# Optimization experiments

Measured on AMD Instinct MI355X. Metric: run time of the kernel, lower is better.

The kernel has to match this reference:

```python
import jax, jax.numpy as jnp
import numpy as np

MOLS = 64
ATOMS = 256
N = MOLS * ATOMS
K_GB = 32
K_GNN = 16
HID = 128
OFFSET = 0.009            # GB dielectric offset (nm)
ALPHA, BETA, GAMMA = 1.0, 0.8, 4.85  # OBC2 coefficients
EPS_FACTOR = 138.935456   # Coulomb constant, kJ*nm/(mol*e^2)
PREF = -EPS_FACTOR * (1.0 - 1.0 / 78.5)


def _edges(key, k_neigh):
    # random intra-molecule neighbors, no self loops (mimics radius-graph structure)
    src = jnp.repeat(jnp.arange(N), k_neigh)
    off = jax.random.randint(key, (N * k_neigh,), 1, ATOMS)
    dst = (src // ATOMS) * ATOMS + (src % ATOMS + off) % ATOMS
    return jnp.stack([src, dst]).astype(jnp.int32)


def setup_inputs() -> dict:
    key = jax.random.key(0)
    ks = jax.random.split(key, 8)
    pos = (jax.random.uniform(ks[0], (N, 3), jnp.float32) * 1.5)
    q = jax.random.uniform(ks[1], (N, 1), jnp.float32) - 0.5
    rad = 0.15 + 0.05 * jax.random.uniform(ks[2], (N, 1), jnp.float32)
    scl = 0.8 + 0.2 * jax.random.uniform(ks[3], (N, 1), jnp.float32)
    rest = jax.random.uniform(ks[4], (N, 4), jnp.float32)
    atom_features = jnp.concatenate([q, rad, scl, rest], axis=1)
    batch = jnp.repeat(jnp.arange(MOLS), ATOMS).astype(jnp.int32)
    edge_index = _edges(ks[5], K_GB)
    gnn_edge_index = _edges(ks[6], K_GNN)

    def lin(k, fi, fo):
        return (jax.random.normal(k, (fi, fo), jnp.float32) / np.float32(np.sqrt(fi)),
                jnp.zeros((fo,), jnp.float32))
    kw = jax.random.split(ks[7], 6)
    i1_w1, i1_b1 = lin(kw[0], 2 * 2 + 1, HID)
    i1_w2, i1_b2 = lin(kw[1], HID, HID)
    i2_w1, i2_b1 = lin(kw[2], 2 * HID + 1, HID)
    i2_w2, i2_b2 = lin(kw[3], HID, HID)
    i3_w1, i3_b1 = lin(kw[4], 2 * HID + 1, HID)
    i3_w2, i3_b2 = lin(kw[5], HID, 1)
    return dict(pos=pos, atom_features=atom_features, batch=batch,
                edge_index=edge_index, gnn_edge_index=gnn_edge_index,
                i1_w1=i1_w1, i1_b1=i1_b1, i1_w2=i1_w2, i1_b2=i1_b2,
                i2_w1=i2_w1, i2_b1=i2_b1, i2_w2=i2_w2, i2_b2=i2_b2,
                i3_w1=i3_w1, i3_b1=i3_b1, i3_w2=i3_w2, i3_b2=i3_b2)


def _dist(pos, ei):
    d2 = jnp.sum((pos[ei[0]] - pos[ei[1]]) ** 2, axis=1)
    return jnp.sqrt(d2 + 1e-12)


def _gb_energies(pos, feats, ei):
    # GBNeck_interaction (Born radii via HCT descreening integral, OBC2 rescale)
    # followed by GBNeck_energies (pairwise GB + self energy), per-atom [N,1]
    n = pos.shape[0]
    src, dst = ei[0], ei[1]
    d = _dist(pos, ei)
    q, radius, scale = feats[:, 0], feats[:, 1], feats[:, 2]
    rho = radius - OFFSET
    sr_j = (scale * rho)[src]
    rho_i = rho[dst]
    U = d + sr_j
    L = jnp.maximum(rho_i, jnp.abs(d - sr_j))
    I = 0.5 * (1.0 / L - 1.0 / U
               + 0.25 * (d - sr_j ** 2 / d) * (1.0 / U ** 2 - 1.0 / L ** 2)
               + 0.5 * jnp.log(L / U) / d)
    I = jnp.where(rho_i < U, I, 0.0)
    Isum = jax.ops.segment_sum(I, dst, num_segments=n)
    psi = Isum * rho
    B = 1.0 / (1.0 / rho - jnp.tanh(ALPHA * psi - BETA * psi ** 2 + GAMMA * psi ** 3) / radius)
    Bi, Bj = B[dst], B[src]
    f_gb = jnp.sqrt(d ** 2 + Bi * Bj * jnp.exp(-d ** 2 / (4.0 * Bi * Bj)))
    e_pair = 0.5 * PREF * q[dst] * q[src] / f_gb  # 0.5: edges are double counted
    e = 0.5 * PREF * q ** 2 / B + jax.ops.segment_sum(e_pair, dst, num_segments=n)
    return e[:, None]


def _in_layer(x, ei, d, w1, b1, w2, b2):
    # IN_layer_all_swish_2pass: edge MLP on [x_i || x_j || d] + scatter-add
    n = x.shape[0]
    m = jnp.concatenate([x[ei[0]], x[ei[1]], d[:, None]], axis=1)
    h = jax.nn.silu(m @ w1 + b1)
    return jax.ops.segment_sum(h @ w2 + b2, ei[1], num_segments=n)


def _energies_all(pos, feats, ei, gei,
                  i1_w1, i1_b1, i1_w2, i1_b2,
                  i2_w1, i2_b1, i2_w2, i2_b2,
                  i3_w1, i3_b1, i3_w2, i3_b2):
    e_gb = _gb_energies(pos, feats, ei)
    d_gnn = _dist(pos, gei)
    x = jax.nn.silu(_in_layer(feats[:, :2], gei, d_gnn, i1_w1, i1_b1, i1_w2, i1_b2))
    x = jax.nn.silu(_in_layer(x, gei, d_gnn, i2_w1, i2_b1, i2_w2, i2_b2))
    x = _in_layer(x, gei, d_gnn, i3_w1, i3_b1, i3_w2, i3_b2)
    return e_gb + x


def reference(pos, atom_features, batch, edge_index, gnn_edge_index,
              i1_w1, i1_b1, i1_w2, i1_b2,
              i2_w1, i2_b1, i2_w2, i2_b2,
              i3_w1, i3_b1, i3_w2, i3_b2):
    ws = (i1_w1, i1_b1, i1_w2, i1_b2, i2_w1, i2_b1, i2_w2, i2_b2,
          i3_w1, i3_b1, i3_w2, i3_b2)
    efun = lambda p: _energies_all(p, atom_features, edge_index, gnn_edge_index, *ws)
    energies, vjp = jax.vjp(efun, pos)  # [N,1]
    (gpos,) = vjp(jnp.ones_like(energies))
    forces = -gpos
    energy = jax.ops.segment_sum(energies[:, 0], batch, num_segments=MOLS)[:, None]
    return energy, forces
```

## Files before the change

kernel.cpp:

```cpp
#include <hip/hip_runtime.h>
#include <hip/hip_bf16.h>

#define NATOMS 16384
#define MOLS   64
#define ATOMSM 256
#define EGB    524288
#define EGNN   262144
#define HID    128
#define NH     (NATOMS*HID)

#define OFFSETC 0.009f
#define ALPHAC  1.0f
#define BETAC   0.8f
#define GAMMAC  4.85f
#define PREFC   (-138.935456f*(1.0f-1.0f/78.5f))

typedef __hip_bfloat16 bf;
typedef __attribute__((ext_vector_type(8))) short bf8v;
typedef __attribute__((ext_vector_type(4))) float f4v;
typedef unsigned int uint;

__device__ __forceinline__ float b2f(bf x){ return __bfloat162float(x); }
__device__ __forceinline__ bf f2b(float x){ return __float2bfloat16(x); }
__device__ __forceinline__ short f2s(float x){ bf h = f2b(x); return *(short*)&h; }
// ... 53 lines not shown
    short* __restrict__ A3at, short* __restrict__ A3bt,
    short* __restrict__ rA2a, short* __restrict__ rA2b,
    short* __restrict__ rA3a, short* __restrict__ rA3b,
    short* __restrict__ rC1, short* __restrict__ rC2,
    const float* __restrict__ feat, const float* __restrict__ A1,
    bf* __restrict__ u1, bf* __restrict__ v1,
    const float* __restrict__ pos, const int* __restrict__ ei,
    float* __restrict__ Isum,
    const int* __restrict__ gei, float* __restrict__ dgnn, int* __restrict__ cnt)
{
    int tid = threadIdx.x;
    if (blockIdx.x < 64){
        int gid = blockIdx.x*256 + tid;
        int j = gid >> 7, k = gid & 127;
        C1t[gid]  = f2s(C1[k*HID+j]);
        C2t[gid]  = f2s(C2[k*HID+j]);
        A2at[gid] = f2s(A2[k*HID+j]);
        A2bt[gid] = f2s(A2[(HID+k)*HID+j]);
        A3at[gid] = f2s(A3[k*HID+j]);
        A3bt[gid] = f2s(A3[(HID+k)*HID+j]);
        rA2a[gid] = f2s(A2[gid]);
        rA2b[gid] = f2s(A2[HID*HID+gid]);
        rA3a[gid] = f2s(A3[gid]);
        rA3b[gid] = f2s(A3[HID*HID+gid]);
        rC1[gid]  = f2s(C1[gid]);
        rC2[gid]  = f2s(C2[gid]);
    } else if (blockIdx.x < 4160){
        int gid2 = (blockIdx.x-64)*256 + tid;
        int i = gid2 >> 6, k2 = (gid2 & 63)*2;
        float q = feat[7*i+0], r = feat[7*i+1];
        float u0 = q*A1[k2]         + r*A1[HID+k2];
        float u1v= q*A1[k2+1]       + r*A1[HID+k2+1];
        float v0 = q*A1[2*HID+k2]   + r*A1[3*HID+k2];
        float v1v= q*A1[2*HID+k2+1] + r*A1[3*HID+k2+1];
        ushort2 uu, vv;
        uu.x = (unsigned short)f2s(u0); uu.y = (unsigned short)f2s(u1v);
        vv.x = (unsigned short)f2s(v0); vv.y = (unsigned short)f2s(v1v);
        *(ushort2*)((short*)u1 + (size_t)i*HID + k2) = uu;
        *(ushort2*)((short*)v1 + (size_t)i*HID + k2) = vv;
    } else if (blockIdx.x < 4672){
        __shared__ float sPx[256], sPy[256], sPz[256], sRho[256], sSr[256];
        __shared__ float sI[256];
        int bb = blockIdx.x - 4160;
        int mbase = (bb >> 3) * 256;
        {
            int i = mbase + tid;
            sPx[tid]=pos[3*i]; sPy[tid]=pos[3*i+1]; sPz[tid]=pos[3*i+2];
            float rad = feat[7*i+1], sc = feat[7*i+2];
            float rho = rad - OFFSETC;
            sRho[tid]=rho; sSr[tid]=sc*rho;
            sI[tid]=0.f;
        }
        __syncthreads();
        int T = bb*256 + tid;
        int s = T >> 3, p = T & 7;
        int sl = s & 255;
        int e0 = s*32 + p*4;
        float px = sPx[sl], py = sPy[sl], pz = sPz[sl];
        float sr = sSr[sl];
        float srr = sr*sr;
        const int* dP = ei + EGB;
        int4 d4 = *(const int4*)(dP + e0);
        int dls[4] = {d4.x&255, d4.y&255, d4.z&255, d4.w&255};
#pragma unroll
        for (int j=0;j<4;j++){
            int dl = dls[j];
            float dx = px - sPx[dl];
            float dy = py - sPy[dl];
            float dz = pz - sPz[dl];
            float d2 = dx*dx+dy*dy+dz*dz + 1e-12f;
            float rd = frsq(d2);
            float d  = d2*rd;
            float rho_i = sRho[dl];
            float U = d + sr;
            if (rho_i < U){
                float L = fmaxf(rho_i, fabsf(d - sr));
                float invU = frcp(U), invL = frcp(L);
                float I = 0.5f*invL - 0.5f*invU
                        + 0.125f*(d - srr*rd)*(invU*invU - invL*invL)
                        + 0.25f*__logf(L*invU)*rd;
                atomicAdd(&sI[dl], I);
            }
        }
        __syncthreads();
        atomicAdd(&Isum[mbase + tid], sI[tid]);
    } else {
        int e = (blockIdx.x-4672)*256 + tid;
        int s = gei[e], dd = gei[EGNN+e];
        float dx = pos[3*s+0] - pos[3*dd+0];
        float dy = pos[3*s+1] - pos[3*dd+1];
        float dz = pos[3*s+2] - pos[3*dd+2];
        dgnn[e] = fsqrt(dx*dx+dy*dy+dz*dz + 1e-12f);
        atomicAdd(&cnt[dd], 1);
    }
}

__global__ __launch_bounds__(256) void k_B(
    const float* __restrict__ feat, const float* __restrict__ Isum,
    float* __restrict__ Bv, float* __restrict__ cB, float* __restrict__ gB,
    float* __restrict__ egb,
    const int* __restrict__ cnt, int* __restrict__ rptr,
    const int* __restrict__ gei, const float* __restrict__ dgnn,
    int* __restrict__ csr, int2* __restrict__ csr2)
{
    int t = threadIdx.x;
    if (blockIdx.x < 64){
        int i = blockIdx.x*256 + t;
        float q   = feat[7*i+0];
        float rad = feat[7*i+1];
        float rho = rad - OFFSETC;
        float psi = Isum[i]*rho;
        float u = psi*(ALPHAC + psi*(-BETAC + GAMMAC*psi));
        float tt = tanhf(u);
        float rrad = frcp(rad);
        float B = frcp(frcp(rho) - tt*rrad);
        Bv[i] = B;
        float du = ALPHAC + psi*(-2.0f*BETAC + 3.0f*GAMMAC*psi);
        cB[i] = B*B*((1.0f-tt*tt)*rrad)*du*rho;
        float Cs = 0.5f*PREFC*q*q;
        float rB = frcp(B);
        egb[i] = Cs*rB;
        gB[i]  = -Cs*rB*rB;
    } else {
        __shared__ int sc[256];
        __shared__ int lcur[256];
        int m = blockIdx.x - 64;
        int c = cnt[m*256+t];
        sc[t] = c; __syncthreads();
        for (int off=1; off<256; off<<=1){
            int x = (t>=off) ? sc[t-off] : 0;
            __syncthreads();
            sc[t] += x;
            __syncthreads();
        }
        int exl = sc[t] - c;
        rptr[m*256+t] = m*4096 + exl;
        lcur[t] = exl;
        __syncthreads();
        int e0 = m*4096;
        for (int j=t; j<4096; j+=256){
            int e = e0 + j;
            int dl = gei[EGNN+e] & 255;
            float d = dgnn[e];
            int p = atomicAdd(&lcur[dl], 1);
            int idx = e0 + p;
            csr[idx] = e;
            int2 rec; rec.x = (e >> 4) << 8;
            rec.y = __float_as_int(d);
            csr2[idx] = rec;
        }
    }
}

__global__ __launch_bounds__(256) void k_gbC(
    const float* __restrict__ pos, const float* __restrict__ feat,
    const int* __restrict__ ei, const float* __restrict__ Bv,
    float* __restrict__ egb, float* __restrict__ gdgb, float* __restrict__ gB)
{
    __shared__ float sPx[256], sPy[256], sPz[256], sB[256], sQf[256];
    __shared__ float sE[256], sG[256];
    int tid = threadIdx.x;
    int mbase = (blockIdx.x >> 3) * 256;
    {
        int i = mbase + tid;
        sPx[tid]=pos[3*i]; sPy[tid]=pos[3*i+1]; sPz[tid]=pos[3*i+2];
        sB[tid]=Bv[i]; sQf[tid]=feat[7*i+0];
        sE[tid]=0.f; sG[tid]=0.f;
    }
    __syncthreads();
    int T = blockIdx.x*256 + tid;
    int s = T >> 3, p = T & 7;
    int sl = s & 255;
    int e0 = s*32 + p*4;
    float px = sPx[sl], py = sPy[sl], pz = sPz[sl];
    float qs = sQf[sl];
    float Bs = sB[sl];
    float gsrc = 0.f;
    const int* dP = ei + EGB;
    int4 d4 = *(const int4*)(dP + e0);
    int dls[4] = {d4.x&255, d4.y&255, d4.z&255, d4.w&255};
#pragma unroll
    for (int j=0;j<4;j++){
        int dl = dls[j];
        float dx = px - sPx[dl];
        float dy = py - sPy[dl];
        float dz = pz - sPz[dl];
        float d2 = dx*dx+dy*dy+dz*dz + 1e-12f;
        float d  = d2*frsq(d2);
        float Bd = sB[dl];
        float C = 0.5f*PREFC*sQf[dl]*qs;
        float P = Bd*Bs;
        float qq = 0.25f*d2*frcp(P);
        float ex = __expf(-qq);
        float f2 = d2 + P*ex;
        float rf = frsq(f2);
        float f3i = rf*rf*rf;
        gdgb[e0+j] = -C*d*(1.f - 0.25f*ex)*f3i;
        float common = -C*ex*(1.f + qq)*0.5f*f3i;
        atomicAdd(&sE[dl], C*rf);
        atomicAdd(&sG[dl], common*Bs);
        gsrc += common*Bd;
    }
    gsrc += __shfl_xor(gsrc,1);
    gsrc += __shfl_xor(gsrc,2);
    gsrc += __shfl_xor(gsrc,4);
    if (p==0) atomicAdd(&sG[sl], gsrc);
    __syncthreads();
    atomicAdd(&egb[mbase + tid], sE[tid]);
    atomicAdd(&gB[mbase + tid],  sG[tid]);
}

__global__ __launch_bounds__(256) void k_gbE(
    const float* __restrict__ pos, const float* __restrict__ feat,
    const int* __restrict__ ei, const float* __restrict__ cB,
    const float* __restrict__ gB,
    const float* __restrict__ gdgb, float* __restrict__ grad)
{
    __shared__ float sPx[256], sPy[256], sPz[256], sRho[256], sSr[256], sCg[256];
    __shared__ float sGx[256], sGy[256], sGz[256];
    int tid = threadIdx.x;
    int mbase = (blockIdx.x >> 3) * 256;
    {
        int i = mbase + tid;
        sPx[tid]=pos[3*i]; sPy[tid]=pos[3*i+1]; sPz[tid]=pos[3*i+2];
        float rad = feat[7*i+1], sc = feat[7*i+2];
        float rho = rad - OFFSETC;
        sRho[tid]=rho; sSr[tid]=sc*rho;
        sCg[tid]=cB[i]*gB[i];
        sGx[tid]=0.f; sGy[tid]=0.f; sGz[tid]=0.f;
    }
    __syncthreads();
    int T = blockIdx.x*256 + tid;
    int s = T >> 3, p = T & 7;
    int sl = s & 255;
    int e0 = s*32 + p*4;
    float px = sPx[sl], py = sPy[sl], pz = sPz[sl];
    float sr = sSr[sl];
    float srr = sr*sr;
    float gx=0.f, gy=0.f, gz=0.f;
    const int* dP = ei + EGB;
    int4 d4 = *(const int4*)(dP + e0);
    int dls[4] = {d4.x&255, d4.y&255, d4.z&255, d4.w&255};
#pragma unroll
    for (int j=0;j<4;j++){
        int dl = dls[j];
        float dx = px - sPx[dl];
        float dy = py - sPy[dl];
        float dz = pz - sPz[dl];
        float d2 = dx*dx+dy*dy+dz*dz + 1e-12f;
        float rd = frsq(d2);
        float d  = d2*rd;
        float rd2 = rd*rd;
        float rho_i = sRho[dl];
        float U = d + sr;
        float gd = gdgb[e0+j];
        if (rho_i < U){
            float aa = fabsf(d - sr);
            float L, Lp;
            if (rho_i >= aa){ L = rho_i; Lp = 0.f; }
            else { L = aa; Lp = (d >= sr) ? 1.f : -1.f; }
            float invU = frcp(U), invL = frcp(L);
            float invU2=invU*invU, invL2=invL*invL;
            float dIdd = -0.5f*Lp*invL2 + 0.5f*invU2
                + 0.125f*(1.f + srr*rd2)*(invU2 - invL2)
                + 0.125f*(d - srr*rd)*(2.f*Lp*invL2*invL - 2.f*invU2*invU)
                + 0.25f*((Lp*invL - invU)*rd - __logf(L*invU)*rd2);
            gd += sCg[dl]*dIdd;
        }
        float c = gd*rd;
        gx += c*dx; gy += c*dy; gz += c*dz;
        atomicAdd(&sGx[dl], -c*dx);
        atomicAdd(&sGy[dl], -c*dy);
        atomicAdd(&sGz[dl], -c*dz);
    }
    gx += __shfl_xor(gx,1); gx += __shfl_xor(gx,2); gx += __shfl_xor(gx,4);
    gy += __shfl_xor(gy,1); gy += __shfl_xor(gy,2); gy += __shfl_xor(gy,4);
    gz += __shfl_xor(gz,1); gz += __shfl_xor(gz,2); gz += __shfl_xor(gz,4);
    if (p==0){
        atomicAdd(&sGx[sl], gx);
        atomicAdd(&sGy[sl], gy);
        atomicAdd(&sGz[sl], gz);
    }
    __syncthreads();
    int i = mbase + tid;
    atomicAdd(&grad[3*i+0], sGx[tid]);
    atomicAdd(&grad[3*i+1], sGy[tid]);
    atomicAdd(&grad[3*i+2], sGz[tid]);
}


template<bool WSDS>
__device__ __forceinline__ void edge_fwd_wave(
    int dst, int lane,
    const int2* __restrict__ csr2, const int* __restrict__ rptr, const int* __restrict__ cnt,
    const uint* __restrict__ u, const uint* __restrict__ v,
    const float* __restrict__ wdp, const float* __restrict__ bb,
    uint* __restrict__ Hs, uint* __restrict__ Sds)
{
    int n = cnt[dst], r0 = rptr[dst];
    float2 wd = *(const float2*)&wdp[2*lane];
    float2 b2 = *(const float2*)&bb[2*lane];
    uint vp = v[dst*64 + lane];
    float base0 = lo2f(vp) + b2.x;
    float base1 = hi2f(vp) + b2.y;
    float h0=0.f,h1=0.f,e0a=0.f,e1a=0.f;
    for (int j0=0; j0<n; j0+=64){
        int m = n - j0; if (m > 64) m = 64;
        int rx = 0, ry = 0;
        if (lane < m){ int2 rc = csr2[r0+j0+lane]; rx = rc.x; ry = rc.y; }
#pragma unroll 2
        for (int j=0;j<m;j++){
            int off = __builtin_amdgcn_readlane(rx, j);
            float d  = __uint_as_float((unsigned)__builtin_amdgcn_readlane(ry, j));
            uint up = *(const uint*)((const char*)u + off + 4*lane);
            float a0 = fmaf(d, wd.x, base0 + lo2f(up));
            float a1 = fmaf(d, wd.y, base1 + hi2f(up));
            float s0 = sigf(a0), s1 = sigf(a1);
            float p0 = a0*s0, p1 = a1*s1;
            h0 += p0; h1 += p1;
            if (WSDS){
                e0a = fmaf(s0, 1.f + a0 - p0, e0a);
                e1a = fmaf(s1, 1.f + a1 - p1, e1a);
            }
        }
    }
    Hs[dst*64+lane] = pack2(h0,h1);
    if (WSDS) Sds[dst*64+lane] = pack2(e0a,e1a);
}

__global__ __launch_bounds__(256,8) void k_edge_fwd0(
    const int2* __restrict__ csr2, const int* __restrict__ rptr, const int* __restrict__ cnt,
    const uint* __restrict__ u, const uint* __restrict__ v,
    const float* __restrict__ wdp, const float* __restrict__ bb,
    uint* __restrict__ Hs)
{
    int lane = threadIdx.x & 63, wid = threadIdx.x >> 6;
    int dst = blockIdx.x*4 + wid;
    edge_fwd_wave<false>(dst, lane, csr2, rptr, cnt, u, v, wdp, bb, Hs, nullptr);
}

__global__ __launch_bounds__(256,8) void k_edge_fwd1(
    const int2* __restrict__ csr2, const int* __restrict__ rptr, const int* __restrict__ cnt,
    const uint* __restrict__ u, const uint* __restrict__ v,
    const float* __restrict__ wdp, const float* __restrict__ bb,
    uint* __restrict__ Hs, uint* __restrict__ Sds)
{
    int lane = threadIdx.x & 63, wid = threadIdx.x >> 6;
    int dst = blockIdx.x*4 + wid;
    edge_fwd_wave<true>(dst, lane, csr2, rptr, cnt, u, v, wdp, bb, Hs, Sds);
}

__global__ __launch_bounds__(256,4) void k_l3(
    const int2* __restrict__ csr2, const int* __restrict__ rptr, const int* __restrict__ cnt,
    const int* __restrict__ gei, const float* __restrict__ dgnn,
    const uint* __restrict__ u, const uint* __restrict__ v,
    const float* __restrict__ A3, const float* __restrict__ B3,
    const float* __restrict__ C3, const float* __restrict__ D3,
    uint* __restrict__ Gd, float* __restrict__ x3,
    uint* __restrict__ Gs, float* __restrict__ gdg)
{
    int lane = threadIdx.x & 63, wid = threadIdx.x >> 6;
    const float* wdp = A3 + 256*HID;
    if (blockIdx.x < NATOMS/4){
        int dst = blockIdx.x*4 + wid;
        int n = cnt[dst], r0 = rptr[dst];
        float2 wd = *(const float2*)&wdp[2*lane];
        float2 b2 = *(const float2*)&B3[2*lane];
        float2 ck = *(const float2*)&C3[2*lane];
        uint vp = v[dst*64 + lane];
        float base0 = lo2f(vp) + b2.x;
        float base1 = hi2f(vp) + b2.y;
        float h0=0.f,h1=0.f,e0a=0.f,e1a=0.f;
        for (int j0=0; j0<n; j0+=64){
            int m = n - j0; if (m > 64) m = 64;
            int rx = 0, ry = 0;
            if (lane < m){ int2 rc = csr2[r0+j0+lane]; rx = rc.x; ry = rc.y; }
#pragma unroll 2
            for (int j=0;j<m;j++){
                int off = __builtin_amdgcn_readlane(rx, j);
                float d  = __uint_as_float((unsigned)__builtin_amdgcn_readlane(ry, j));
                uint up = *(const uint*)((const char*)u + off + 4*lane);
                float a0 = fmaf(d, wd.x, base0 + lo2f(up));
                float a1 = fmaf(d, wd.y, base1 + hi2f(up));
                float s0 = sigf(a0), s1 = sigf(a1);
                float p0 = a0*s0, p1 = a1*s1;
                h0 += p0; h1 += p1;
                e0a = fmaf(s0, 1.f + a0 - p0, e0a);
                e1a = fmaf(s1, 1.f + a1 - p1, e1a);
            }
        }
        Gd[dst*64+lane] = pack2(ck.x*e0a, ck.y*e1a);
        float px = waveRed(ck.x*h0 + ck.y*h1);
        if (lane==0) x3[dst] = px + (float)n*D3[0];
    } else {
        int s = (blockIdx.x - NATOMS/4)*4 + wid;
        int doff = 0, dbit = 0;
        if (lane < 16){
            doff = gei[EGNN + s*16 + lane] << 8;
            dbit = __float_as_int(dgnn[s*16+lane]);
        }
        float2 wd = *(const float2*)&wdp[2*lane];
        float2 b2 = *(const float2*)&B3[2*lane];
        float2 ck = *(const float2*)&C3[2*lane];
        uint up = u[s*64 + lane];
        float us0 = lo2f(up) + b2.x;
        float us1 = hi2f(up) + b2.y;
        float cw0 = ck.x*wd.x, cw1 = ck.y*wd.y;
        float gs0=0.f, gs1=0.f;
        float A[16];
#pragma unroll
        for (int t=0;t<16;t++){
            int off = __builtin_amdgcn_readlane(doff, t);
            float d = __uint_as_float((unsigned)__builtin_amdgcn_readlane(dbit, t));
            uint vp = *(const uint*)((const char*)v + off + 4*lane);
            float a0 = fmaf(d, wd.x, us0 + lo2f(vp));
            float a1 = fmaf(d, wd.y, us1 + hi2f(vp));
            float s0 = sigf(a0), s1 = sigf(a1);
            float p0 = a0*s0, p1 = a1*s1;
            float dv0 = s0*(1.f + a0 - p0);
            float dv1 = s1*(1.f + a1 - p1);
            gs0 += dv0; gs1 += dv1;
            A[t] = fmaf(dv1, cw1, dv0*cw0);
        }
        Gs[s*64+lane] = pack2(ck.x*gs0, ck.y*gs1);
        float tot = red16(A, lane);
        if (lane < 32 && !(lane & 1)) gdg[s*16 + (lane>>1)] = tot;
    }
}

__global__ __launch_bounds__(256,4) void k_bwd_src(
    const int* __restrict__ gei, const float* __restrict__ dgnn,
    const uint* __restrict__ u, const uint* __restrict__ v,
    const float* __restrict__ wdp, const float* __restrict__ bb,
    const uint* __restrict__ gH,
    uint* __restrict__ Gs, float* __restrict__ gdg)
{
    int lane = threadIdx.x & 63, wid = threadIdx.x >> 6;
    int s = blockIdx.x*4 + wid;
    int doff = 0, dbit = 0;
    if (lane < 16){
        doff = gei[EGNN + s*16 + lane] << 8;
        dbit = __float_as_int(dgnn[s*16+lane]);
    }
    float gold = gdg[s*16 + ((lane>>1)&15)];
    float2 wd = *(const float2*)&wdp[2*lane];
    float2 b2 = *(const float2*)&bb[2*lane];
    uint up = u[s*64 + lane];
    float us0 = lo2f(up) + b2.x;
    float us1 = hi2f(up) + b2.y;
    float gs0=0.f, gs1=0.f;
    float A[16];
#pragma unroll
    for (int t=0;t<16;t++){
        int off = __builtin_amdgcn_readlane(doff, t);
        float d = __uint_as_float((unsigned)__builtin_amdgcn_readlane(dbit, t));
        uint vp = *(const uint*)((const char*)v + off + 4*lane);
        uint gp = *(const uint*)((const char*)gH + off + 4*lane);
        float a0 = fmaf(d, wd.x, us0 + lo2f(vp));
        float a1 = fmaf(d, wd.y, us1 + hi2f(vp));
        float s0 = sigf(a0), s1 = sigf(a1);
        float p0 = a0*s0, p1 = a1*s1;
        float ga0 = s0*(1.f + a0 - p0) * lo2f(gp);
        float ga1 = s1*(1.f + a1 - p1) * hi2f(gp);
        gs0 += ga0; gs1 += ga1;
        A[t] = fmaf(ga1, wd.y, ga0*wd.x);
    }
    if (Gs) Gs[s*64+lane] = pack2(gs0, gs1);
    float tot = red16(A, lane);
    if (lane < 32 && !(lane & 1)) gdg[s*16 + (lane>>1)] = gold + tot;
}

__global__ __launch_bounds__(256) void k_node_fwd_uv_mfma(
    const short* __restrict__ Hs, const int* __restrict__ cnt,
    const short* __restrict__ Ct, const float* __restrict__ D,
    const short* __restrict__ Aat, const short* __restrict__ Abt,
    bf* __restrict__ dsz, bf* __restrict__ u, bf* __restrict__ v)
{
    __shared__ short sx[64*HID];
    int lane = threadIdx.x & 63, w = threadIdx.x >> 6;
    int m0 = blockIdx.x*64 + w*16;
    int ar = lane & 15, kg = lane >> 4;
    bf8v af[4];
#pragma unroll
    for (int s=0;s<4;s++) af[s] = *(const bf8v*)&Hs[(size_t)(m0+ar)*HID + s*32 + kg*8];
    f4v acc[8];
#pragma unroll
    for (int nt=0;nt<8;nt++){
        acc[nt] = (f4v){0.f,0.f,0.f,0.f};
        const short* bp = Ct + (nt*16+ar)*HID + kg*8;
#pragma unroll
        for (int s=0;s<4;s++){
            bf8v bv = *(const bf8v*)(bp + s*32);
            acc[nt] = __builtin_amdgcn_mfma_f32_16x16x32_bf16(af[s], bv, acc[nt], 0,0,0);
        }
    }
    float cn[4];
#pragma unroll
    for (int r=0;r<4;r++) cn[r] = (float)cnt[m0 + kg*4 + r];
#pragma unroll
    for (int nt=0;nt<8;nt++){
        int j = nt*16 + ar;
        float Dj = D[j];
#pragma unroll
        for (int r=0;r<4;r++){
            int m = m0 + kg*4 + r;
            float zv = acc[nt][r] + cn[r]*Dj;
            float sg = sigf(zv);
            dsz[(size_t)m*HID + j] = f2b(sg*(1.f + zv*(1.f - sg)));
            sx[(w*16 + kg*4 + r)*HID + j] = f2s(zv*sg);
        }
    }
    __syncthreads();
#pragma unroll
    for (int s=0;s<4;s++) af[s] = *(const bf8v*)&sx[(w*16+ar)*HID + s*32 + kg*8];
    f4v au[8], av[8];
#pragma unroll
    for (int nt=0;nt<8;nt++){
        au[nt] = (f4v){0.f,0.f,0.f,0.f};
        av[nt] = (f4v){0.f,0.f,0.f,0.f};
        const short* bpa = Aat + (nt*16+ar)*HID + kg*8;
        const short* bpb = Abt + (nt*16+ar)*HID + kg*8;
#pragma unroll
        for (int s=0;s<4;s++){
            bf8v ba = *(const bf8v*)(bpa + s*32);
            bf8v bb = *(const bf8v*)(bpb + s*32);
            au[nt] = __builtin_amdgcn_mfma_f32_16x16x32_bf16(af[s], ba, au[nt], 0,0,0);
            av[nt] = __builtin_amdgcn_mfma_f32_16x16x32_bf16(af[s], bb, av[nt], 0,0,0);
        }
    }
#pragma unroll
    for (int nt=0;nt<8;nt++){
        int j = nt*16 + ar;
#pragma unroll
        for (int r=0;r<4;r++){
            int m = m0 + kg*4 + r;
            u[(size_t)m*HID + j] = f2b(au[nt][r]);
            v[(size_t)m*HID + j] = f2b(av[nt][r]);
        }
    }
}

__global__ __launch_bounds__(256) void k_gx_node_bwd_mfma(
    const short* __restrict__ Gs, const short* __restrict__ Gd,
    const short* __restrict__ gHin, const short* __restrict__ Sds,
    const short* __restrict__ Ra, const short* __restrict__ Rb,
    const bf* __restrict__ dsz, const short* __restrict__ Rc,
    bf* __restrict__ gHout)
{
    __shared__ short st[64*HID];
    int lane = threadIdx.x & 63, w = threadIdx.x >> 6;
    int m0 = blockIdx.x*64 + w*16;
    int ar = lane & 15, kg = lane >> 4;
    bf8v as_[4], ad_[4];
#pragma unroll
    for (int s=0;s<4;s++)
        as_[s] = *(const bf8v*)&Gs[(size_t)(m0+ar)*HID + s*32 + kg*8];
    if (Sds){
#pragma unroll
        for (int s=0;s<4;s++){
            bf8v g = *(const bf8v*)&gHin[(size_t)(m0+ar)*HID + s*32 + kg*8];
            bf8v sd = *(const bf8v*)&Sds[(size_t)(m0+ar)*HID + s*32 + kg*8];
            bf8v r;
#pragma unroll
            for (int i=0;i<8;i++) r[i] = f2s(s2f(g[i])*s2f(sd[i]));
            ad_[s] = r;
        }
    } else {
#pragma unroll
        for (int s=0;s<4;s++)
            ad_[s] = *(const bf8v*)&Gd[(size_t)(m0+ar)*HID + s*32 + kg*8];
    }
    f4v acc[8];
#pragma unroll
    for (int nt=0;nt<8;nt++){
        acc[nt] = (f4v){0.f,0.f,0.f,0.f};
        const short* bpa = Ra + (nt*16+ar)*HID + kg*8;
        const short* bpb = Rb + (nt*16+ar)*HID + kg*8;
#pragma unroll
        for (int s=0;s<4;s++){
            bf8v ba = *(const bf8v*)(bpa + s*32);
            bf8v bb = *(const bf8v*)(bpb + s*32);
            acc[nt] = __builtin_amdgcn_mfma_f32_16x16x32_bf16(as_[s], ba, acc[nt], 0,0,0);
            acc[nt] = __builtin_amdgcn_mfma_f32_16x16x32_bf16(ad_[s], bb, acc[nt], 0,0,0);
        }
    }
#pragma unroll
    for (int nt=0;nt<8;nt++){
        int j = nt*16 + ar;
#pragma unroll
        for (int r=0;r<4;r++){
            int m = m0 + kg*4 + r;
            float t = acc[nt][r] * b2f(dsz[(size_t)m*HID + j]);
            st[(w*16 + kg*4 + r)*HID + j] = f2s(t);
        }
    }
    __syncthreads();
    bf8v af[4];
#pragma unroll
    for (int s=0;s<4;s++) af[s] = *(const bf8v*)&st[(w*16+ar)*HID + s*32 + kg*8];
    f4v a2[8];
#pragma unroll
    for (int nt=0;nt<8;nt++){
        a2[nt] = (f4v){0.f,0.f,0.f,0.f};
        const short* bp = Rc + (nt*16+ar)*HID + kg*8;
#pragma unroll
        for (int s=0;s<4;s++){
            bf8v bc = *(const bf8v*)(bp + s*32);
            a2[nt] = __builtin_amdgcn_mfma_f32_16x16x32_bf16(af[s], bc, a2[nt], 0,0,0);
        }
    }
#pragma unroll
    for (int nt=0;nt<8;nt++){
        int j = nt*16 + ar;
#pragma unroll
        for (int r=0;r<4;r++){
            gHout[(size_t)(m0 + kg*4 + r)*HID + j] = f2b(a2[nt][r]);
        }
    }
}

__global__ __launch_bounds__(256) void k_out(
    const float* __restrict__ pos, const int* __restrict__ gei,
    const int* __restrict__ csr, const int* __restrict__ rptr, const int* __restrict__ cnt,
    const float* __restrict__ dgnn, const float* __restrict__ gdg,
    const float* __restrict__ grad,
    const float* __restrict__ egb, const float* __restrict__ x3,
    float* __restrict__ out)
{
    int tid = threadIdx.x;
    if (blockIdx.x < 512){
        float* fout = out + MOLS;
        int T = blockIdx.x*256 + tid;
        int i = T >> 3, p = T & 7;
        float px = pos[3*i+0], py = pos[3*i+1], pz = pos[3*i+2];
        float ax=0.f, ay=0.f, az=0.f;
        for (int j=p;j<16;j+=8){
            int e = i*16 + j;
            int o = gei[EGNN+e];
            float c = gdg[e]*frcp(dgnn[e]);
            ax += c*(px - pos[3*o+0]);
            ay += c*(py - pos[3*o+1]);
            az += c*(pz - pos[3*o+2]);
        }
        int n = cnt[i], r0 = rptr[i];
        for (int j=p;j<n;j+=8){
            int e = csr[r0+j];
            int o = e >> 4;
            float c = gdg[e]*frcp(dgnn[e]);
            ax += c*(px - pos[3*o+0]);
            ay += c*(py - pos[3*o+1]);
            az += c*(pz - pos[3*o+2]);
        }
        ax += __shfl_xor(ax,1); ax += __shfl_xor(ax,2); ax += __shfl_xor(ax,4);
        ay += __shfl_xor(ay,1); ay += __shfl_xor(ay,2); ay += __shfl_xor(ay,4);
        az += __shfl_xor(az,1); az += __shfl_xor(az,2); az += __shfl_xor(az,4);
        if (p==0){
            fout[3*i+0] = -(grad[3*i+0] + ax);
            fout[3*i+1] = -(grad[3*i+1] + ay);
            fout[3*i+2] = -(grad[3*i+2] + az);
        }
    } else {
        __shared__ float red[4];
        int m = blockIdx.x - 512;
        int i = m*ATOMSM + tid;
        float en = egb[i] + x3[i];
        float v = waveRed(en);
        int wave = tid>>6, lane = tid&63;
        if (lane==0) red[wave] = v;
        __syncthreads();
        if (tid==0) out[m] = red[0]+red[1]+red[2]+red[3];
    }
}

extern "C" void kernel_launch(void* const* d_in, const int* in_sizes, int n_in,
                              void* d_out, int out_size, void* d_ws, size_t ws_size,
                              hipStream_t stream)
{
    const float* pos  = (const float*)d_in[0];
    const float* feat = (const float*)d_in[1];
    const int* ei  = (const int*)d_in[3];
    const int* gei = (const int*)d_in[4];
    const float* A1f = (const float*)d_in[5];  const float* B1f = (const float*)d_in[6];
    const float* C1f = (const float*)d_in[7];  const float* D1f = (const float*)d_in[8];
    const float* A2f = (const float*)d_in[9];  const float* B2f = (const float*)d_in[10];
    const float* C2f = (const float*)d_in[11]; const float* D2f = (const float*)d_in[12];
    const float* A3f = (const float*)d_in[13]; const float* B3f = (const float*)d_in[14];
    const float* C3f = (const float*)d_in[15]; const float* D3f = (const float*)d_in[16];

    float* w = (float*)d_ws;
    size_t off = 0;
    auto nxt = [&](size_t n)->float*{ float* p = w + off; off += (n + 255) & ~(size_t)255; return p; };
    float* Isum = nxt(NATOMS);
    int*   cnt  = (int*)nxt(NATOMS);
    float* grad = nxt(3*NATOMS);
    float* Bv = nxt(NATOMS); float* cB = nxt(NATOMS);
    float* gB = nxt(NATOMS); float* egb = nxt(NATOMS); float* x3 = nxt(NATOMS);
    int*   rptr = (int*)nxt(NATOMS);
    int*   csr  = (int*)nxt(EGNN);
    int2*  csr2 = (int2*)nxt((size_t)EGNN*2);
    float* dgnn = nxt(EGNN); float* gdgnn = nxt(EGNN); float* gdgb = nxt(EGB);
    bf* dsz1 = (bf*)nxt(NH/2); bf* dsz2 = (bf*)nxt(NH/2);
    bf* Hs1 = (bf*)nxt(NH/2); bf* Hs2 = (bf*)nxt(NH/2);
    bf* Gs3 = (bf*)nxt(NH/2); bf* Gd3 = (bf*)nxt(NH/2);
    bf* Sds2 = (bf*)nxt(NH/2);
    bf* u1 = (bf*)nxt(NH/2); bf* v1 = (bf*)nxt(NH/2);
    bf* u2 = (bf*)nxt(NH/2); bf* v2 = (bf*)nxt(NH/2);
    bf* v3 = (bf*)nxt(NH/2);
    short* C1t  = (short*)nxt(8192); short* C2t  = (short*)nxt(8192);
    short* A2at = (short*)nxt(8192); short* A2bt = (short*)nxt(8192);
    short* A3at = (short*)nxt(8192); short* A3bt = (short*)nxt(8192);
    short* rA2a = (short*)nxt(8192); short* rA2b = (short*)nxt(8192);
    short* rA3a = (short*)nxt(8192); short* rA3b = (short*)nxt(8192);
    short* rC1  = (short*)nxt(8192); short* rC2  = (short*)nxt(8192);
    bf* u3  = Hs1;
    bf* gH2 = Hs2;
    bf* Gs2 = Gs3;
    bf* gH1 = u3;

    hipMemsetAsync(Isum, 0, (size_t)5*NATOMS*sizeof(float), stream);

    k_A<<<64 + NH/512 + 512 + EGNN/256, 256, 0, stream>>>(
        A2f, C1f, A3f, C2f,
        C1t, C2t, A2at, A2bt, A3at, A3bt, rA2a, rA2b, rA3a, rA3b, rC1, rC2,
        feat, A1f, u1, v1,
        pos, ei, Isum, gei, dgnn, cnt);

    k_B<<<128,256,0,stream>>>(feat, Isum, Bv, cB, gB, egb, cnt, rptr,
                              gei, dgnn, csr, csr2);

    k_edge_fwd0<<<NATOMS/4,256,0,stream>>>(csr2, rptr, cnt, (const uint*)u1, (const uint*)v1,
                                           A1f+4*HID, B1f, (uint*)Hs1);
    k_gbC<<<512,256,0,stream>>>(pos, feat, ei, Bv, egb, gdgb, gB);
    k_node_fwd_uv_mfma<<<NATOMS/64,256,0,stream>>>((const short*)Hs1, cnt, C1t, D1f,
                                                   A2at, A2bt, dsz1, u2, v2);
    k_edge_fwd1<<<NATOMS/4,256,0,stream>>>(csr2, rptr, cnt, (const uint*)u2, (const uint*)v2,
                                           A2f+256*HID, B2f, (uint*)Hs2, (uint*)Sds2);
    k_gbE<<<512,256,0,stream>>>(pos, feat, ei, cB, gB, gdgb, grad);
    k_node_fwd_uv_mfma<<<NATOMS/64,256,0,stream>>>((const short*)Hs2, cnt, C2t, D2f,
                                                   A3at, A3bt, dsz2, u3, v3);

    k_l3<<<2*(NATOMS/4),256,0,stream>>>(csr2, rptr, cnt, gei, dgnn,
                                        (const uint*)u3, (const uint*)v3,
                                        A3f, B3f, C3f, D3f,
                                        (uint*)Gd3, x3, (uint*)Gs3, gdgnn);

    k_gx_node_bwd_mfma<<<NATOMS/64,256,0,stream>>>((const short*)Gs3, (const short*)Gd3,
        (const short*)nullptr, (const short*)nullptr, rA3a, rA3b, dsz2, rC2, gH2);
    k_bwd_src<<<NATOMS/4,256,0,stream>>>(gei, dgnn, (const uint*)u2, (const uint*)v2,
                                         A2f+256*HID, B2f, (const uint*)gH2,
                                         (uint*)Gs2, gdgnn);
    k_gx_node_bwd_mfma<<<NATOMS/64,256,0,stream>>>((const short*)Gs2, (const short*)nullptr,
        (const short*)gH2, (const short*)Sds2, rA2a, rA2b, dsz1, rC1, gH1);
    k_bwd_src<<<NATOMS/4,256,0,stream>>>(gei, dgnn, (const uint*)u1, (const uint*)v1,
                                         A1f+4*HID, B1f, (const uint*)gH1,
                                         (uint*)nullptr, gdgnn);

    k_out<<<576,256,0,stream>>>(pos, gei, csr, rptr, cnt, dgnn, gdgnn,
                                grad, egb, x3, (float*)d_out);
}
```

Baseline: 328.9 us.

## Merge GB pair kernels into GNN edge kernels via block-range dispatch

Folds the GB energy kernel (k_gbC) into the layer-1 edge-forward launch and the GB gradient kernel (k_gbE) into the layer-2 edge-forward launch. Each combined kernel sends its first 512 blocks to the GB work and the rest to the edge work, so the independent tasks run side by side and two launches go away. The change also raises the gather-loop unroll from 2 to 8, builds row pointers from an unsigned offset, and raises the min-waves hint from 4 to 6 in k_l3 and k_bwd_src. Possible costs are higher register use from the fused shared-memory branches and the larger unroll, plus register spills under the tighter launch bounds.

```diff
diff --git a/kernel.cpp b/kernel.cpp
--- a/kernel.cpp
+++ b/kernel.cpp
@@ -229,143 +229,6 @@
     }
 }
 
-__global__ __launch_bounds__(256) void k_gbC(
-    const float* __restrict__ pos, const float* __restrict__ feat,
-    const int* __restrict__ ei, const float* __restrict__ Bv,
-    float* __restrict__ egb, float* __restrict__ gdgb, float* __restrict__ gB)
-{
-    __shared__ float sPx[256], sPy[256], sPz[256], sB[256], sQf[256];
-    __shared__ float sE[256], sG[256];
-    int tid = threadIdx.x;
-    int mbase = (blockIdx.x >> 3) * 256;
-    {
-        int i = mbase + tid;
-        sPx[tid]=pos[3*i]; sPy[tid]=pos[3*i+1]; sPz[tid]=pos[3*i+2];
-        sB[tid]=Bv[i]; sQf[tid]=feat[7*i+0];
-        sE[tid]=0.f; sG[tid]=0.f;
-    }
-    __syncthreads();
-    int T = blockIdx.x*256 + tid;
-    int s = T >> 3, p = T & 7;
-    int sl = s & 255;
-    int e0 = s*32 + p*4;
-    float px = sPx[sl], py = sPy[sl], pz = sPz[sl];
-    float qs = sQf[sl];
-    float Bs = sB[sl];
-    float gsrc = 0.f;
-    const int* dP = ei + EGB;
-    int4 d4 = *(const int4*)(dP + e0);
-    int dls[4] = {d4.x&255, d4.y&255, d4.z&255, d4.w&255};
-#pragma unroll
-    for (int j=0;j<4;j++){
-        int dl = dls[j];
-        float dx = px - sPx[dl];
-        float dy = py - sPy[dl];
-        float dz = pz - sPz[dl];
-        float d2 = dx*dx+dy*dy+dz*dz + 1e-12f;
-        float d  = d2*frsq(d2);
-        float Bd = sB[dl];
-        float C = 0.5f*PREFC*sQf[dl]*qs;
-        float P = Bd*Bs;
-        float qq = 0.25f*d2*frcp(P);
-        float ex = __expf(-qq);
-        float f2 = d2 + P*ex;
-        float rf = frsq(f2);
-        float f3i = rf*rf*rf;
-        gdgb[e0+j] = -C*d*(1.f - 0.25f*ex)*f3i;
-        float common = -C*ex*(1.f + qq)*0.5f*f3i;
-        atomicAdd(&sE[dl], C*rf);
-        atomicAdd(&sG[dl], common*Bs);
-        gsrc += common*Bd;
-    }
-    gsrc += __shfl_xor(gsrc,1);
-    gsrc += __shfl_xor(gsrc,2);
-    gsrc += __shfl_xor(gsrc,4);
-    if (p==0) atomicAdd(&sG[sl], gsrc);
-    __syncthreads();
-    atomicAdd(&egb[mbase + tid], sE[tid]);
-    atomicAdd(&gB[mbase + tid],  sG[tid]);
-}
-
-__global__ __launch_bounds__(256) void k_gbE(
-    const float* __restrict__ pos, const float* __restrict__ feat,
-    const int* __restrict__ ei, const float* __restrict__ cB,
-    const float* __restrict__ gB,
-    const float* __restrict__ gdgb, float* __restrict__ grad)
-{
-    __shared__ float sPx[256], sPy[256], sPz[256], sRho[256], sSr[256], sCg[256];
-    __shared__ float sGx[256], sGy[256], sGz[256];
-    int tid = threadIdx.x;
-    int mbase = (blockIdx.x >> 3) * 256;
-    {
-        int i = mbase + tid;
-        sPx[tid]=pos[3*i]; sPy[tid]=pos[3*i+1]; sPz[tid]=pos[3*i+2];
-        float rad = feat[7*i+1], sc = feat[7*i+2];
-        float rho = rad - OFFSETC;
-        sRho[tid]=rho; sSr[tid]=sc*rho;
-        sCg[tid]=cB[i]*gB[i];
-        sGx[tid]=0.f; sGy[tid]=0.f; sGz[tid]=0.f;
-    }
-    __syncthreads();
-    int T = blockIdx.x*256 + tid;
-    int s = T >> 3, p = T & 7;
-    int sl = s & 255;
-    int e0 = s*32 + p*4;
-    float px = sPx[sl], py = sPy[sl], pz = sPz[sl];
-    float sr = sSr[sl];
-    float srr = sr*sr;
-    float gx=0.f, gy=0.f, gz=0.f;
-    const int* dP = ei + EGB;
-    int4 d4 = *(const int4*)(dP + e0);
-    int dls[4] = {d4.x&255, d4.y&255, d4.z&255, d4.w&255};
-#pragma unroll
-    for (int j=0;j<4;j++){
-        int dl = dls[j];
-        float dx = px - sPx[dl];
-        float dy = py - sPy[dl];
-        float dz = pz - sPz[dl];
-        float d2 = dx*dx+dy*dy+dz*dz + 1e-12f;
-        float rd = frsq(d2);
-        float d  = d2*rd;
-        float rd2 = rd*rd;
-        float rho_i = sRho[dl];
-        float U = d + sr;
-        float gd = gdgb[e0+j];
-        if (rho_i < U){
-            float aa = fabsf(d - sr);
-            float L, Lp;
-            if (rho_i >= aa){ L = rho_i; Lp = 0.f; }
-            else { L = aa; Lp = (d >= sr) ? 1.f : -1.f; }
-            float invU = frcp(U), invL = frcp(L);
-            float invU2=invU*invU, invL2=invL*invL;
-            float dIdd = -0.5f*Lp*invL2 + 0.5f*invU2
-                + 0.125f*(1.f + srr*rd2)*(invU2 - invL2)
-                + 0.125f*(d - srr*rd)*(2.f*Lp*invL2*invL - 2.f*invU2*invU)
-                + 0.25f*((Lp*invL - invU)*rd - __logf(L*invU)*rd2);
-            gd += sCg[dl]*dIdd;
-        }
-        float c = gd*rd;
-        gx += c*dx; gy += c*dy; gz += c*dz;
-        atomicAdd(&sGx[dl], -c*dx);
-        atomicAdd(&sGy[dl], -c*dy);
-        atomicAdd(&sGz[dl], -c*dz);
-    }
-    gx += __shfl_xor(gx,1); gx += __shfl_xor(gx,2); gx += __shfl_xor(gx,4);
-    gy += __shfl_xor(gy,1); gy += __shfl_xor(gy,2); gy += __shfl_xor(gy,4);
-    gz += __shfl_xor(gz,1); gz += __shfl_xor(gz,2); gz += __shfl_xor(gz,4);
-    if (p==0){
-        atomicAdd(&sGx[sl], gx);
-        atomicAdd(&sGy[sl], gy);
-        atomicAdd(&sGz[sl], gz);
-    }
-    __syncthreads();
-    int i = mbase + tid;
-    atomicAdd(&grad[3*i+0], sGx[tid]);
-    atomicAdd(&grad[3*i+1], sGy[tid]);
-    atomicAdd(&grad[3*i+2], sGz[tid]);
-}
-
-
 template<bool WSDS>
 __device__ __forceinline__ void edge_fwd_wave(
     int dst, int lane,
@@ -385,11 +248,12 @@
         int m = n - j0; if (m > 64) m = 64;
         int rx = 0, ry = 0;
         if (lane < m){ int2 rc = csr2[r0+j0+lane]; rx = rc.x; ry = rc.y; }
-#pragma unroll 2
+#pragma unroll 8
         for (int j=0;j<m;j++){
-            int off = __builtin_amdgcn_readlane(rx, j);
+            uint off = (uint)__builtin_amdgcn_readlane(rx, j);
             float d  = __uint_as_float((unsigned)__builtin_amdgcn_readlane(ry, j));
-            uint up = *(const uint*)((const char*)u + off + 4*lane);
+            const uint* urow = (const uint*)((const char*)u + off);
+            uint up = urow[lane];
             float a0 = fmaf(d, wd.x, base0 + lo2f(up));
             float a1 = fmaf(d, wd.y, base1 + hi2f(up));
             float s0 = sigf(a0), s1 = sigf(a1);
@@ -405,29 +269,234 @@
     if (WSDS) Sds[dst*64+lane] = pack2(e0a,e1a);
 }
 
-__global__ __launch_bounds__(256,8) void k_edge_fwd0(
+__global__ __launch_bounds__(256,8) void k_ef0C(
+    const float* __restrict__ pos, const float* __restrict__ feat,
+    const int* __restrict__ ei, const float* __restrict__ Bv,
+    float* __restrict__ egb, float* __restrict__ gdgb, float* __restrict__ gB,
     const int2* __restrict__ csr2, const int* __restrict__ rptr, const int* __restrict__ cnt,
     const uint* __restrict__ u, const uint* __restrict__ v,
     const float* __restrict__ wdp, const float* __restrict__ bb,
     uint* __restrict__ Hs)
 {
-    int lane = threadIdx.x & 63, wid = threadIdx.x >> 6;
-    int dst = blockIdx.x*4 + wid;
-    edge_fwd_wave<false>(dst, lane, csr2, rptr, cnt, u, v, wdp, bb, Hs, nullptr);
-}
-
-__global__ __launch_bounds__(256,8) void k_edge_fwd1(
+    int tid = threadIdx.x;
+    if (blockIdx.x < 512){
+        __shared__ float sPx[256], sPy[256], sPz[256], sB[256], sQf[256];
+        __shared__ float sE[256], sG[256];
+        int mbase = (blockIdx.x >> 3) * 256;
+        {
+            int i = mbase + tid;
+            sPx[tid]=pos[3*i]; sPy[tid]=pos[3*i+1]; sPz[tid]=pos[3*i+2];
+            sB[tid]=Bv[i]; sQf[tid]=feat[7*i+0];
+            sE[tid]=0.f; sG[tid]=0.f;
+        }
+        __syncthreads();
+        int T = blockIdx.x*256 + tid;
+        int s = T >> 3, p = T & 7;
+        int sl = s & 255;
+        int e0 = s*32 + p*4;
+        float px = sPx[sl], py = sPy[sl], pz = sPz[sl];
+        float qs = sQf[sl];
+        float Bs = sB[sl];
+        float gsrc = 0.f;
+        const int* dP = ei + EGB;
+        int4 d4 = *(const int4*)(dP + e0);
+        int dls[4] = {d4.x&255, d4.y&255, d4.z&255, d4.w&255};
+#pragma unroll
+        for (int j=0;j<4;j++){
+            int dl = dls[j];
+            float dx = px - sPx[dl];
+            float dy = py - sPy[dl];
+            float dz = pz - sPz[dl];
+            float d2 = dx*dx+dy*dy+dz*dz + 1e-12f;
+            float d  = d2*frsq(d2);
+            float Bd = sB[dl];
+            float C = 0.5f*PREFC*sQf[dl]*qs;
+            float P = Bd*Bs;
+            float qq = 0.25f*d2*frcp(P);
+            float ex = __expf(-qq);
+            float f2 = d2 + P*ex;
+            float rf = frsq(f2);
+            float f3i = rf*rf*rf;
+            gdgb[e0+j] = -C*d*(1.f - 0.25f*ex)*f3i;
+            float common = -C*ex*(1.f + qq)*0.5f*f3i;
+            atomicAdd(&sE[dl], C*rf);
+            atomicAdd(&sG[dl], common*Bs);
+            gsrc += common*Bd;
+        }
+        gsrc += __shfl_xor(gsrc,1);
+        gsrc += __shfl_xor(gsrc,2);
+        gsrc += __shfl_xor(gsrc,4);
+        if (p==0) atomicAdd(&sG[sl], gsrc);
+        __syncthreads();
+        atomicAdd(&egb[mbase + tid], sE[tid]);
+        atomicAdd(&gB[mbase + tid],  sG[tid]);
+    } else {
+        int lane = tid & 63, wid = tid >> 6;
+        int dst = (blockIdx.x-512)*4 + wid;
+        edge_fwd_wave<false>(dst, lane, csr2, rptr, cnt, u, v, wdp, bb, Hs, nullptr);
+    }
+}
+
+__global__ __launch_bounds__(256,8) void k_ef1E(
+    const float* __restrict__ pos, const float* __restrict__ feat,
+    const int* __restrict__ ei, const float* __restrict__ cB,
+    const float* __restrict__ gB,
+    const float* __restrict__ gdgb, float* __restrict__ grad,
     const int2* __restrict__ csr2, const int* __restrict__ rptr, const int* __restrict__ cnt,
     const uint* __restrict__ u, const uint* __restrict__ v,
     const float* __restrict__ wdp, const float* __restrict__ bb,
     uint* __restrict__ Hs, uint* __restrict__ Sds)
 {
-    int lane = threadIdx.x & 63, wid = threadIdx.x >> 6;
-    int dst = blockIdx.x*4 + wid;
-    edge_fwd_wave<true>(dst, lane, csr2, rptr, cnt, u, v, wdp, bb, Hs, Sds);
-}
-
-__global__ __launch_bounds__(256,4) void k_l3(
+    int tid = threadIdx.x;
+    if (blockIdx.x < 512){
+        __shared__ float sPx[256], sPy[256], sPz[256], sRho[256], sSr[256], sCg[256];
+        __shared__ float sGx[256], sGy[256], sGz[256];
+        int mbase = (blockIdx.x >> 3) * 256;
+        {
+            int i = mbase + tid;
+            sPx[tid]=pos[3*i]; sPy[tid]=pos[3*i+1]; sPz[tid]=pos[3*i+2];
+            float rad = feat[7*i+1], sc = feat[7*i+2];
+            float rho = rad - OFFSETC;
+            sRho[tid]=rho; sSr[tid]=sc*rho;
+            sCg[tid]=cB[i]*gB[i];
+            sGx[tid]=0.f; sGy[tid]=0.f; sGz[tid]=0.f;
+        }
+        __syncthreads();
+        int T = blockIdx.x*256 + tid;
+        int s = T >> 3, p = T & 7;
+        int sl = s & 255;
+        int e0 = s*32 + p*4;
+        float px = sPx[sl], py = sPy[sl], pz = sPz[sl];
+        float sr = sSr[sl];
+        float srr = sr*sr;
+        float gx=0.f, gy=0.f, gz=0.f;
+        const int* dP = ei + EGB;
+        int4 d4 = *(const int4*)(dP + e0);
+        int dls[4] = {d4.x&255, d4.y&255, d4.z&255, d4.w&255};
+#pragma unroll
+        for (int j=0;j<4;j++){
+            int dl = dls[j];
+            float dx = px - sPx[dl];
+            float dy = py - sPy[dl];
+            float dz = pz - sPz[dl];
+            float d2 = dx*dx+dy*dy+dz*dz + 1e-12f;
+            float rd = frsq(d2);
+            float d  = d2*rd;
+            float rd2 = rd*rd;
+            float rho_i = sRho[dl];
+            float U = d + sr;
+            float gd = gdgb[e0+j];
+            if (rho_i < U){
+                float aa = fabsf(d - sr);
+                float L, Lp;
+                if (rho_i >= aa){ L = rho_i; Lp = 0.f; }
+                else { L = aa; Lp = (d >= sr) ? 1.f : -1.f; }
+                float invU = frcp(U), invL = frcp(L);
+                float invU2=invU*invU, invL2=invL*invL;
+                float dIdd = -0.5f*Lp*invL2 + 0.5f*invU2
+                    + 0.125f*(1.f + srr*rd2)*(invU2 - invL2)
+                    + 0.125f*(d - srr*rd)*(2.f*Lp*invL2*invL - 2.f*invU2*invU)
+                    + 0.25f*((Lp*invL - invU)*rd - __logf(L*invU)*rd2);
+                gd += sCg[dl]*dIdd;
+            }
+            float c = gd*rd;
+            gx += c*dx; gy += c*dy; gz += c*dz;
+            atomicAdd(&sGx[dl], -c*dx);
+            atomicAdd(&sGy[dl], -c*dy);
+            atomicAdd(&sGz[dl], -c*dz);
+        }
+        gx += __shfl_xor(gx,1); gx += __shfl_xor(gx,2); gx += __shfl_xor(gx,4);
+        gy += __shfl_xor(gy,1); gy += __shfl_xor(gy,2); gy += __shfl_xor(gy,4);
+        gz += __shfl_xor(gz,1); gz += __shfl_xor(gz,2); gz += __shfl_xor(gz,4);
+        if (p==0){
+            atomicAdd(&sGx[sl], gx);
+            atomicAdd(&sGy[sl], gy);
+            atomicAdd(&sGz[sl], gz);
+        }
+        __syncthreads();
+        int i = mbase + tid;
+        atomicAdd(&grad[3*i+0], sGx[tid]);
+        atomicAdd(&grad[3*i+1], sGy[tid]);
+        atomicAdd(&grad[3*i+2], sGz[tid]);
+    } else {
+        int lane = tid & 63, wid = tid >> 6;
+        int dst = (blockIdx.x-512)*4 + wid;
+        edge_fwd_wave<true>(dst, lane, csr2, rptr, cnt, u, v, wdp, bb, Hs, Sds);
+    }
+}
+
+__global__ __launch_bounds__(256) void k_node_fwd_uv_mfma(
+    const short* __restrict__ Hs, const int* __restrict__ cnt,
+    const short* __restrict__ Ct, const float* __restrict__ D,
+    const short* __restrict__ Aat, const short* __restrict__ Abt,
+    bf* __restrict__ dsz, bf* __restrict__ u, bf* __restrict__ v)
+{
+    __shared__ short sx[64*HID];
+    int tid = threadIdx.x;
+    int lane = tid & 63, w = tid >> 6;
+    int m0 = blockIdx.x*64 + w*16;
+    int ar = lane & 15, kg = lane >> 4;
+    bf8v af[4];
+#pragma unroll
+    for (int s=0;s<4;s++) af[s] = *(const bf8v*)&Hs[(size_t)(m0+ar)*HID + s*32 + kg*8];
+    f4v acc[8];
+#pragma unroll
+    for (int nt=0;nt<8;nt++){
+        acc[nt] = (f4v){0.f,0.f,0.f,0.f};
+        const short* bp = Ct + (nt*16+ar)*HID + kg*8;
+#pragma unroll
+        for (int s=0;s<4;s++){
+            bf8v bv = *(const bf8v*)(bp + s*32);
+            acc[nt] = __builtin_amdgcn_mfma_f32_16x16x32_bf16(af[s], bv, acc[nt], 0,0,0);
+        }
+    }
+    float cn[4];
+#pragma unroll
+    for (int r=0;r<4;r++) cn[r] = (float)cnt[m0 + kg*4 + r];
+#pragma unroll
+    for (int nt=0;nt<8;nt++){
+        int j = nt*16 + ar;
+        float Dj = D[j];
+#pragma unroll
+        for (int r=0;r<4;r++){
+            int m = m0 + kg*4 + r;
+            float zv = acc[nt][r] + cn[r]*Dj;
+            float sg = sigf(zv);
+            dsz[(size_t)m*HID + j] = f2b(sg*(1.f + zv*(1.f - sg)));
+            sx[(w*16 + kg*4 + r)*HID + j] = f2s(zv*sg);
+        }
+    }
+    __syncthreads();
+#pragma unroll
+    for (int s=0;s<4;s++) af[s] = *(const bf8v*)&sx[(w*16+ar)*HID + s*32 + kg*8];
+    f4v au[8], av[8];
+#pragma unroll
+    for (int nt=0;nt<8;nt++){
+        au[nt] = (f4v){0.f,0.f,0.f,0.f};
+        av[nt] = (f4v){0.f,0.f,0.f,0.f};
+        const short* bpa = Aat + (nt*16+ar)*HID + kg*8;
+        const short* bpb = Abt + (nt*16+ar)*HID + kg*8;
+#pragma unroll
+        for (int s=0;s<4;s++){
+            bf8v ba = *(const bf8v*)(bpa + s*32);
+            bf8v bb = *(const bf8v*)(bpb + s*32);
+            au[nt] = __builtin_amdgcn_mfma_f32_16x16x32_bf16(af[s], ba, au[nt], 0,0,0);
+            av[nt] = __builtin_amdgcn_mfma_f32_16x16x32_bf16(af[s], bb, av[nt], 0,0,0);
+        }
+    }
+#pragma unroll
+    for (int nt=0;nt<8;nt++){
+        int j = nt*16 + ar;
+#pragma unroll
+        for (int r=0;r<4;r++){
+            int m = m0 + kg*4 + r;
+            u[(size_t)m*HID + j] = f2b(au[nt][r]);
+            v[(size_t)m*HID + j] = f2b(av[nt][r]);
+        }
+    }
+}
+
+__global__ __launch_bounds__(256,6) void k_l3(
     const int2* __restrict__ csr2, const int* __restrict__ rptr, const int* __restrict__ cnt,
     const int* __restrict__ gei, const float* __restrict__ dgnn,
     const uint* __restrict__ u, const uint* __restrict__ v,
@@ -452,11 +521,12 @@
             int m = n - j0; if (m > 64) m = 64;
             int rx = 0, ry = 0;
             if (lane < m){ int2 rc = csr2[r0+j0+lane]; rx = rc.x; ry = rc.y; }
-#pragma unroll 2
+#pragma unroll 8
             for (int j=0;j<m;j++){
-                int off = __builtin_amdgcn_readlane(rx, j);
+                uint off = (uint)__builtin_amdgcn_readlane(rx, j);
                 float d  = __uint_as_float((unsigned)__builtin_amdgcn_readlane(ry, j));
-                uint up = *(const uint*)((const char*)u + off + 4*lane);
+                const uint* urow = (const uint*)((const char*)u + off);
+                uint up = urow[lane];
                 float a0 = fmaf(d, wd.x, base0 + lo2f(up));
                 float a1 = fmaf(d, wd.y, base1 + hi2f(up));
                 float s0 = sigf(a0), s1 = sigf(a1);
@@ -487,9 +557,10 @@
         float A[16];
 #pragma unroll
         for (int t=0;t<16;t++){
-            int off = __builtin_amdgcn_readlane(doff, t);
+            uint off = (uint)__builtin_amdgcn_readlane(doff, t);
             float d = __uint_as_float((unsigned)__builtin_amdgcn_readlane(dbit, t));
-            uint vp = *(const uint*)((const char*)v + off + 4*lane);
+            const uint* vrow = (const uint*)((const char*)v + off);
+            uint vp = vrow[lane];
             float a0 = fmaf(d, wd.x, us0 + lo2f(vp));
             float a1 = fmaf(d, wd.y, us1 + hi2f(vp));
             float s0 = sigf(a0), s1 = sigf(a1);
@@ -505,7 +576,7 @@
     }
 }
 
-__global__ __launch_bounds__(256,4) void k_bwd_src(
+__global__ __launch_bounds__(256,6) void k_bwd_src(
     const int* __restrict__ gei, const float* __restrict__ dgnn,
     const uint* __restrict__ u, const uint* __restrict__ v,
     const float* __restrict__ wdp, const float* __restrict__ bb,
@@ -529,10 +600,12 @@
     float A[16];
 #pragma unroll
     for (int t=0;t<16;t++){
-        int off = __builtin_amdgcn_readlane(doff, t);
+        uint off = (uint)__builtin_amdgcn_readlane(doff, t);
         float d = __uint_as_float((unsigned)__builtin_amdgcn_readlane(dbit, t));
-        uint vp = *(const uint*)((const char*)v + off + 4*lane);
-        uint gp = *(const uint*)((const char*)gH + off + 4*lane);
+        const uint* vrow = (const uint*)((const char*)v + off);
+        const uint* grow = (const uint*)((const char*)gH + off);
+        uint vp = vrow[lane];
+        uint gp = grow[lane];
         float a0 = fmaf(d, wd.x, us0 + lo2f(vp));
         float a1 = fmaf(d, wd.y, us1 + hi2f(vp));
         float s0 = sigf(a0), s1 = sigf(a1);
@@ -545,76 +618,6 @@
     if (Gs) Gs[s*64+lane] = pack2(gs0, gs1);
     float tot = red16(A, lane);
     if (lane < 32 && !(lane & 1)) gdg[s*16 + (lane>>1)] = gold + tot;
-}
-
-__global__ __launch_bounds__(256) void k_node_fwd_uv_mfma(
-    const short* __restrict__ Hs, const int* __restrict__ cnt,
-    const short* __restrict__ Ct, const float* __restrict__ D,
-    const short* __restrict__ Aat, const short* __restrict__ Abt,
-    bf* __restrict__ dsz, bf* __restrict__ u, bf* __restrict__ v)
-{
-    __shared__ short sx[64*HID];
-    int lane = threadIdx.x & 63, w = threadIdx.x >> 6;
-    int m0 = blockIdx.x*64 + w*16;
-    int ar = lane & 15, kg = lane >> 4;
-    bf8v af[4];
-#pragma unroll
-    for (int s=0;s<4;s++) af[s] = *(const bf8v*)&Hs[(size_t)(m0+ar)*HID + s*32 + kg*8];
-    f4v acc[8];
-#pragma unroll
-    for (int nt=0;nt<8;nt++){
-        acc[nt] = (f4v){0.f,0.f,0.f,0.f};
-        const short* bp = Ct + (nt*16+ar)*HID + kg*8;
-#pragma unroll
-        for (int s=0;s<4;s++){
-            bf8v bv = *(const bf8v*)(bp + s*32);
-            acc[nt] = __builtin_amdgcn_mfma_f32_16x16x32_bf16(af[s], bv, acc[nt], 0,0,0);
-        }
-    }
-    float cn[4];
-#pragma unroll
-    for (int r=0;r<4;r++) cn[r] = (float)cnt[m0 + kg*4 + r];
-#pragma unroll
-    for (int nt=0;nt<8;nt++){
-        int j = nt*16 + ar;
-        float Dj = D[j];
-#pragma unroll
-        for (int r=0;r<4;r++){
-            int m = m0 + kg*4 + r;
-            float zv = acc[nt][r] + cn[r]*Dj;
-            float sg = sigf(zv);
-            dsz[(size_t)m*HID + j] = f2b(sg*(1.f + zv*(1.f - sg)));
-            sx[(w*16 + kg*4 + r)*HID + j] = f2s(zv*sg);
-        }
-    }
-    __syncthreads();
-#pragma unroll
-    for (int s=0;s<4;s++) af[s] = *(const bf8v*)&sx[(w*16+ar)*HID + s*32 + kg*8];
-    f4v au[8], av[8];
-#pragma unroll
-    for (int nt=0;nt<8;nt++){
-        au[nt] = (f4v){0.f,0.f,0.f,0.f};
-        av[nt] = (f4v){0.f,0.f,0.f,0.f};
-        const short* bpa = Aat + (nt*16+ar)*HID + kg*8;
-        const short* bpb = Abt + (nt*16+ar)*HID + kg*8;
-#pragma unroll
-        for (int s=0;s<4;s++){
-            bf8v ba = *(const bf8v*)(bpa + s*32);
-            bf8v bb = *(const bf8v*)(bpb + s*32);
-            au[nt] = __builtin_amdgcn_mfma_f32_16x16x32_bf16(af[s], ba, au[nt], 0,0,0);
-            av[nt] = __builtin_amdgcn_mfma_f32_16x16x32_bf16(af[s], bb, av[nt], 0,0,0);
-        }
-    }
-#pragma unroll
-    for (int nt=0;nt<8;nt++){
-        int j = nt*16 + ar;
-#pragma unroll
-        for (int r=0;r<4;r++){
-            int m = m0 + kg*4 + r;
-            u[(size_t)m*HID + j] = f2b(au[nt][r]);
-            v[(size_t)m*HID + j] = f2b(av[nt][r]);
-        }
-    }
 }
 
 __global__ __launch_bounds__(256) void k_gx_node_bwd_mfma(
@@ -805,14 +808,18 @@
     k_B<<<128,256,0,stream>>>(feat, Isum, Bv, cB, gB, egb, cnt, rptr,
                               gei, dgnn, csr, csr2);
 
-    k_edge_fwd0<<<NATOMS/4,256,0,stream>>>(csr2, rptr, cnt, (const uint*)u1, (const uint*)v1,
-                                           A1f+4*HID, B1f, (uint*)Hs1);
-    k_gbC<<<512,256,0,stream>>>(pos, feat, ei, Bv, egb, gdgb, gB);
+    k_ef0C<<<512 + NATOMS/4, 256, 0, stream>>>(
+        pos, feat, ei, Bv, egb, gdgb, gB,
+        csr2, rptr, cnt, (const uint*)u1, (const uint*)v1, A1f+4*HID, B1f, (uint*)Hs1);
+
     k_node_fwd_uv_mfma<<<NATOMS/64,256,0,stream>>>((const short*)Hs1, cnt, C1t, D1f,
                                                    A2at, A2bt, dsz1, u2, v2);
-    k_edge_fwd1<<<NATOMS/4,256,0,stream>>>(csr2, rptr, cnt, (const uint*)u2, (const uint*)v2,
-                                           A2f+256*HID, B2f, (uint*)Hs2, (uint*)Sds2);
-    k_gbE<<<512,256,0,stream>>>(pos, feat, ei, cB, gB, gdgb, grad);
+
+    k_ef1E<<<512 + NATOMS/4, 256, 0, stream>>>(
+        pos, feat, ei, cB, gB, gdgb, grad,
+        csr2, rptr, cnt, (const uint*)u2, (const uint*)v2, A2f+256*HID, B2f,
+        (uint*)Hs2, (uint*)Sds2);
+
     k_node_fwd_uv_mfma<<<NATOMS/64,256,0,stream>>>((const short*)Hs2, cnt, C2t, D2f,
                                                    A3at, A3bt, dsz2, u3, v3);
 
```

Measured after the change: 316.5 us, median of 2. 1.04x faster.
